# Optimization experiments

Measured on AMD Instinct MI355X. Metric: run time of the kernel, lower is better.

Reference implementation:

```python
import jax, jax.numpy as jnp
import numpy as np

N = 100_000   # num destination nodes (adj rows)
M = 100_000   # num source/neighbor nodes (adj cols)
E = 3_200_000 # num edges (avg degree 32)
D_IN = 128
DIM = 128
LEAKY_ALPHA = 0.2  # tf.nn.leaky_relu default


def setup_inputs() -> dict:
    key = jax.random.key(0)
    ks = jax.random.split(key, 7)
    return {
        "self_embedding": jax.random.normal(ks[0], (N, D_IN), jnp.float32),
        "neigh_embedding": jax.random.normal(ks[1], (M, D_IN), jnp.float32),
        "W": jax.random.normal(ks[2], (D_IN, DIM), jnp.float32) / np.sqrt(D_IN).astype(np.float32),
        "w_self": jax.random.normal(ks[3], (DIM, 1), jnp.float32) * 0.1,
        "w_neigh": jax.random.normal(ks[4], (DIM, 1), jnp.float32) * 0.1,
        "edge_row": jax.random.randint(ks[5], (E,), 0, N, jnp.int32),
        "edge_col": jax.random.randint(ks[6], (E,), 0, M, jnp.int32),
    }


def reference(self_embedding, neigh_embedding, W, w_self, w_neigh, edge_row, edge_col):
    # Dense projections (shared weight, no bias)
    from_all = neigh_embedding @ W    # [M, DIM]
    from_self = self_embedding @ W    # [N, DIM]

    # Per-node attention logits
    self_weight = (from_self @ w_self)[:, 0]   # [N]
    all_weight = (from_all @ w_neigh)[:, 0]    # [M]

    # Per-edge score: leaky_relu(self_weight[row] + all_weight[col])
    scores = jax.nn.leaky_relu(self_weight[edge_row] + all_weight[edge_col],
                               negative_slope=LEAKY_ALPHA)  # [E]

    n = self_embedding.shape[0]
    # Sparse (segment) softmax over each row's edges, numerically stable
    row_max = jax.ops.segment_max(scores, edge_row, num_segments=n)
    row_max = jnp.where(jnp.isfinite(row_max), row_max, 0.0)  # guard empty rows
    e = jnp.exp(scores - row_max[edge_row])
    denom = jax.ops.segment_sum(e, edge_row, num_segments=n)
    denom = jnp.where(denom > 0, denom, 1.0)
    alpha = e / denom[edge_row]  # [E]

    # Sparse-dense matmul: output[i] = sum_j alpha_ij * from_all[j]
    agg = jax.ops.segment_sum(alpha[:, None] * from_all[edge_col], edge_row,
                              num_segments=n)  # [N, DIM]

    # renorm=False path: residual with from_self, then activation
    return jax.nn.relu(from_self + agg)
```

## Files before the change

### kernel.cpp

```cpp
#include <hip/hip_runtime.h>
#include <math.h>

#define DIM 128
#define LEAKY 0.2f
#define CAP 80
#define RPB 128
#define NBMAX 1024
#define PART_CHUNK 4096

typedef __attribute__((ext_vector_type(8))) short short8_t;
typedef __attribute__((ext_vector_type(8))) __bf16 bf16x8;
typedef __attribute__((ext_vector_type(4))) float f32x4;

__device__ __forceinline__ unsigned short f32_to_bf16_bits(float x) {
  unsigned u = __float_as_uint(x);
  u += 0x7fffu + ((u >> 16) & 1u);
  return (unsigned short)(u >> 16);
}

__global__ __launch_bounds__(256) void gemm_neigh_q(
    const float* __restrict__ emb, const float* __restrict__ W,
    const float* __restrict__ wvec, unsigned char* __restrict__ fa_i8,
    float2* __restrict__ awsc, int nrows)
{
  __shared__ __align__(16) char smem[34816];
  unsigned short* Wt = (unsigned short*)smem;
  int t = threadIdx.x;
  int lane = t & 63;
  int wid = t >> 6;

  for (int i = t; i < 4096; i += 256) {
    int k = i >> 5;
    int c4 = (i & 31) << 2;
    float4 w4 = *(const float4*)(W + k * 128 + c4);
    Wt[(c4 + 0) * 136 + k] = f32_to_bf16_bits(w4.x);
    Wt[(c4 + 1) * 136 + k] = f32_to_bf16_bits(w4.y);
    Wt[(c4 + 2) * 136 + k] = f32_to_bf16_bits(w4.z);
    Wt[(c4 + 3) * 136 + k] = f32_to_bf16_bits(w4.w);
  }
  __syncthreads();

  int row0 = blockIdx.x * 128 + wid * 32;
  bool active = row0 < nrows;
  int lr = lane & 15;
  int lk = lane >> 4;

  f32x4 acc[2][8];
  if (active) {
    bf16x8 a[2][4];
#pragma unroll
    for (int rf = 0; rf < 2; rf++) {
      int row = row0 + rf * 16 + lr;
      row = min(row, nrows - 1);
      const float* src = emb + (size_t)row * DIM;
#pragma unroll
      for (int ks = 0; ks < 4; ks++) {
        int kb = ks * 32 + lk * 8;
        float4 x = *(const float4*)(src + kb);
        float4 y = *(const float4*)(src + kb + 4);
        union { short8_t s; bf16x8 b; } f;
        f.s[0] = (short)f32_to_bf16_bits(x.x); f.s[1] = (short)f32_to_bf16_bits(x.y);
        f.s[2] = (short)f32_to_bf16_bits(x.z); f.s[3] = (short)f32_to_bf16_bits(x.w);
        f.s[4] = (short)f32_to_bf16_bits(y.x); f.s[5] = (short)f32_to_bf16_bits(y.y);
        f.s[6] = (short)f32_to_bf16_bits(y.z); f.s[7] = (short)f32_to_bf16_bits(y.w);
        a[rf][ks] = f.b;
      }
    }
#pragma unroll
    for (int rf = 0; rf < 2; rf++)
#pragma unroll
      for (int cf = 0; cf < 8; cf++)
        acc[rf][cf] = (f32x4){0.f, 0.f, 0.f, 0.f};
#pragma unroll
    for (int ks = 0; ks < 4; ks++) {
#pragma unroll
      for (int cf = 0; cf < 8; cf++) {
        bf16x8 wf = *(const bf16x8*)(Wt + (cf * 16 + lr) * 136 + ks * 32 + lk * 8);
        acc[0][cf] = __builtin_amdgcn_mfma_f32_16x16x32_bf16(a[0][ks], wf, acc[0][cf], 0, 0, 0);
        acc[1][cf] = __builtin_amdgcn_mfma_f32_16x16x32_bf16(a[1][ks], wf, acc[1][cf], 0, 0, 0);
      }
    }
  }
  __syncthreads();

  unsigned char* Q = (unsigned char*)smem + wid * 4096;
  if (active) {
#pragma unroll
    for (int rf = 0; rf < 2; rf++) {
      float pp[4] = {0.f, 0.f, 0.f, 0.f};
#pragma unroll
      for (int cf = 0; cf < 8; cf++) {
        float wvv = wvec[cf * 16 + lr];
#pragma unroll
        for (int r = 0; r < 4; r++) pp[r] += acc[rf][cf][r] * wvv;
      }
#pragma unroll
      for (int r = 0; r < 4; r++) {
        pp[r] += __shfl_xor(pp[r], 1);
        pp[r] += __shfl_xor(pp[r], 2);
        pp[r] += __shfl_xor(pp[r], 4);
        pp[r] += __shfl_xor(pp[r], 8);
      }
      float m[4];
#pragma unroll
      for (int r = 0; r < 4; r++) {
        float mm = 0.f;
#pragma unroll
        for (int cf = 0; cf < 8; cf++) mm = fmaxf(mm, fabsf(acc[rf][cf][r]));
        mm = fmaxf(mm, __shfl_xor(mm, 1));
        mm = fmaxf(mm, __shfl_xor(mm, 2));
        mm = fmaxf(mm, __shfl_xor(mm, 4));
        mm = fmaxf(mm, __shfl_xor(mm, 8));
        m[r] = mm;
      }
#pragma unroll
      for (int r = 0; r < 4; r++) {
        int rl = rf * 16 + lk * 4 + r;
        int row = row0 + rl;
        float inv = m[r] > 0.f ? 127.f / m[r] : 0.f;
        if (row < nrows && lr == 0)
          awsc[row] = make_float2(pp[r], m[r] * (1.f / 127.f));
#pragma unroll
        for (int cf = 0; cf < 8; cf++) {
          int q = (int)__builtin_rintf(acc[rf][cf][r] * inv) + 128;
          Q[rl * 128 + cf * 16 + lr] = (unsigned char)(q & 0xff);
        }
      }
    }
  }
  __syncthreads();

  if (active) {
    unsigned char* dstb = fa_i8 + (size_t)row0 * DIM;
    int nbytes = min(32, nrows - row0) * DIM;
    for (int i = lane * 16; i < 4096; i += 1024) {
      if (i < nbytes)
        *(uint4*)(dstb + i) = *(const uint4*)(Q + i);
    }
  }
}

__global__ __launch_bounds__(256) void gemm_self_f32(
    const float* __restrict__ emb, const float* __restrict__ W,
    const float* __restrict__ wvec, float* __restrict__ out,
    float* __restrict__ wout, int nrows)
{
  __shared__ unsigned short Wt[128 * 136];
  int t = threadIdx.x;
  int lane = t & 63;
  int wid = t >> 6;

  for (int i = t; i < 4096; i += 256) {
    int k = i >> 5;
    int c4 = (i & 31) << 2;
    float4 w4 = *(const float4*)(W + k * 128 + c4);
    Wt[(c4 + 0) * 136 + k] = f32_to_bf16_bits(w4.x);
    Wt[(c4 + 1) * 136 + k] = f32_to_bf16_bits(w4.y);
    Wt[(c4 + 2) * 136 + k] = f32_to_bf16_bits(w4.z);
    Wt[(c4 + 3) * 136 + k] = f32_to_bf16_bits(w4.w);
  }
  __syncthreads();

  int row0 = blockIdx.x * 128 + wid * 32;
  if (row0 >= nrows) return;

  int lr = lane & 15;
  int lk = lane >> 4;

  bf16x8 a[2][4];
#pragma unroll
  for (int rf = 0; rf < 2; rf++) {
    int row = row0 + rf * 16 + lr;
    row = min(row, nrows - 1);
    const float* src = emb + (size_t)row * DIM;
#pragma unroll
    for (int ks = 0; ks < 4; ks++) {
      int kb = ks * 32 + lk * 8;
      float4 x = *(const float4*)(src + kb);
      float4 y = *(const float4*)(src + kb + 4);
      union { short8_t s; bf16x8 b; } f;
      f.s[0] = (short)f32_to_bf16_bits(x.x); f.s[1] = (short)f32_to_bf16_bits(x.y);
      f.s[2] = (short)f32_to_bf16_bits(x.z); f.s[3] = (short)f32_to_bf16_bits(x.w);
      f.s[4] = (short)f32_to_bf16_bits(y.x); f.s[5] = (short)f32_to_bf16_bits(y.y);
      f.s[6] = (short)f32_to_bf16_bits(y.z); f.s[7] = (short)f32_to_bf16_bits(y.w);
      a[rf][ks] = f.b;
    }
  }

  f32x4 acc[2][8];
#pragma unroll
  for (int rf = 0; rf < 2; rf++)
#pragma unroll
    for (int cf = 0; cf < 8; cf++)
      acc[rf][cf] = (f32x4){0.f, 0.f, 0.f, 0.f};

#pragma unroll
  for (int ks = 0; ks < 4; ks++) {
#pragma unroll
    for (int cf = 0; cf < 8; cf++) {
      bf16x8 wf = *(const bf16x8*)(Wt + (cf * 16 + lr) * 136 + ks * 32 + lk * 8);
      acc[0][cf] = __builtin_amdgcn_mfma_f32_16x16x32_bf16(a[0][ks], wf, acc[0][cf], 0, 0, 0);
      acc[1][cf] = __builtin_amdgcn_mfma_f32_16x16x32_bf16(a[1][ks], wf, acc[1][cf], 0, 0, 0);
    }
  }

#pragma unroll
  for (int rf = 0; rf < 2; rf++) {
    float pp[4] = {0.f, 0.f, 0.f, 0.f};
#pragma unroll
    for (int cf = 0; cf < 8; cf++) {
      float wvv = wvec[cf * 16 + lr];
#pragma unroll
      for (int r = 0; r < 4; r++) pp[r] += acc[rf][cf][r] * wvv;
    }
#pragma unroll
    for (int r = 0; r < 4; r++) {
      pp[r] += __shfl_xor(pp[r], 1);
      pp[r] += __shfl_xor(pp[r], 2);
      pp[r] += __shfl_xor(pp[r], 4);
      pp[r] += __shfl_xor(pp[r], 8);
    }
#pragma unroll
    for (int r = 0; r < 4; r++) {
      int row = row0 + rf * 16 + lk * 4 + r;
      if (row < nrows) {
        if (lr == 0) wout[row] = pp[r];
#pragma unroll
        for (int cf = 0; cf < 8; cf++)
          out[(size_t)row * DIM + cf * 16 + lr] = acc[rf][cf][r];
      }
    }
  }
}

__global__ __launch_bounds__(256) void partition_edges(
    const int* __restrict__ erow, const int* __restrict__ ecol,
    unsigned* __restrict__ streams, int capB, int* __restrict__ gcur,
    int E, int nb)
{
  __shared__ int cnt[NBMAX];
  __shared__ int base_[NBMAX];
  __shared__ int pos[NBMAX];
  int t = threadIdx.x;
  for (int i = t; i < nb; i += 256) { cnt[i] = 0; pos[i] = 0; }
  __syncthreads();

  int e0 = blockIdx.x * PART_CHUNK + t * 16;
  int rows[16], cols[16];
#pragma unroll
  for (int q = 0; q < 4; q++) {
    int e = e0 + q * 4;
    if (e + 3 < E) {
      *(int4*)(rows + q * 4) = *(const int4*)(erow + e);
      *(int4*)(cols + q * 4) = *(const int4*)(ecol + e);
    } else {
#pragma unroll
      for (int j = 0; j < 4; j++) {
        rows[q * 4 + j] = (e + j < E) ? erow[e + j] : -1;
        cols[q * 4 + j] = (e + j < E) ? ecol[e + j] : 0;
      }
    }
  }
#pragma unroll
  for (int j = 0; j < 16; j++)
    if (rows[j] >= 0) atomicAdd(&cnt[rows[j] >> 7], 1);
  __syncthreads();
  for (int i = t; i < nb; i += 256)
    base_[i] = cnt[i] ? atomicAdd(gcur + i, cnt[i]) : 0;
  __syncthreads();
#pragma unroll
  for (int j = 0; j < 16; j++) {
    if (rows[j] >= 0) {
      int b = rows[j] >> 7;
      int idx = base_[b] + atomicAdd(&pos[b], 1);
      if (idx < capB)
        streams[(size_t)b * capB + idx] =
            (unsigned)cols[j] | ((unsigned)(rows[j] & (RPB - 1)) << 20);
    }
  }
}

__global__ __launch_bounds__(256) void bucket_scatter(
    const unsigned* __restrict__ streams, int capB,
    const int* __restrict__ gcur,
    const float* __restrict__ sw, const float2* __restrict__ awsc,
    unsigned* __restrict__ perm, int* __restrict__ deg,
    float* __restrict__ invd, int N)
{
  __shared__ __align__(16) unsigned slots[RPB * CAP];
  __shared__ int cnt[RPB];
  __shared__ float dsum[RPB];
  __shared__ float sw_l[RPB];
  int b = blockIdx.x;
  int t = threadIdx.x;
  int row0 = b * RPB;
  if (t < RPB) {
    cnt[t] = 0; dsum[t] = 0.f;
    int row = row0 + t;
    sw_l[t] = (row < N) ? sw[row] : 0.f;
  }
  __syncthreads();

  int n = min(gcur[b], capB);
  const unsigned* s = streams + (size_t)b * capB;
  for (int i = t * 4; i < n; i += 1024) {
    int nv = min(4, n - i);
    unsigned v[4];
    if (nv == 4) {
      uint4 u = *(const uint4*)(s + i);
      v[0] = u.x; v[1] = u.y; v[2] = u.z; v[3] = u.w;
    } else {
      for (int j = 0; j < nv; j++) v[j] = s[i + j];
    }
    unsigned col[4]; int rl[4]; float2 ws[4];
#pragma unroll
    for (int j = 0; j < 4; j++) {
      if (j < nv) {
        col[j] = v[j] & 0xFFFFFu;
        rl[j] = v[j] >> 20;
        ws[j] = awsc[col[j]];
      }
    }
#pragma unroll
    for (int j = 0; j < 4; j++) {
      if (j < nv) {
        float sc = sw_l[rl[j]] + ws[j].x;
        sc = sc > 0.f ? sc : LEAKY * sc;
        float e = __expf(sc);
        atomicAdd(&dsum[rl[j]], e);
        float a = e * ws[j].y;
        unsigned eb = f32_to_bf16_bits(a);
        int p = atomicAdd(&cnt[rl[j]], 1);
        if (p < CAP) slots[rl[j] * CAP + p] = col[j] | (eb << 17);
      }
    }
  }
  __syncthreads();

  unsigned* dst = perm + (size_t)row0 * CAP;
  const int W4 = CAP / 4;
  for (int i = t; i < RPB * W4; i += 256) {
    int rl = i / W4, w = i - rl * W4;
    if (w * 4 < min(cnt[rl], CAP))
      *(uint4*)(dst + rl * CAP + w * 4) = *(const uint4*)(slots + rl * CAP + w * 4);
  }
  if (t < RPB) {
    int row = row0 + t;
    if (row < N) {
      deg[row] = min(cnt[t], CAP);
      float d = dsum[t];
      invd[row] = d > 0.f ? 1.f / d : 1.f;
    }
  }
}

__global__ __launch_bounds__(256) void aggregate_kernel(
    const unsigned char* __restrict__ fa_i8,
    const unsigned* __restrict__ perm, const int* __restrict__ deg_arr,
    const float* __restrict__ invd, float* __restrict__ out, int n)
{
  int wid = threadIdx.x >> 6;
  int lane = threadIdx.x & 63;
  int row = blockIdx.x * 4 + wid;
  if (row >= n) return;
  int deg = deg_arr[row];
  float inv = invd[row];
  size_t base = (size_t)row * CAP;

  int g  = lane >> 3;
  int sl = lane & 7;

  size_t o = (size_t)row * DIM + sl * 16;
  float4 rr0, rr1, rr2, rr3;
  if (g == 0) {
    rr0 = *(const float4*)(out + o);
    rr1 = *(const float4*)(out + o + 4);
    rr2 = *(const float4*)(out + o + 8);
    rr3 = *(const float4*)(out + o + 12);
  }

  float acc[16];
#pragma unroll
  for (int k = 0; k < 16; k++) acc[k] = 0.f;
  float Bl = 0.f;

  for (int bb = 0; bb < deg; bb += 64) {
    int nact = min(64, deg - bb);
    unsigned v = 0;
    if (lane < nact) v = perm[base + bb + lane];

    for (int half = 0; half < 2; half++) {
      if (half * 32 >= nact) break;
#pragma unroll
      for (int jj = 0; jj < 4; jj++) {
        int eidx = half * 32 + (jj << 3) + g;
        unsigned vj = __shfl(v, eidx);
        int   cj = vj & 0x1FFFFu;
        float aj = __uint_as_float((vj >> 17) << 16);
        uint4 u = *(const uint4*)(fa_i8 + (size_t)cj * DIM + sl * 16);
        Bl += aj;
        acc[0]  += aj * (float)( u.x        & 0xffu);
        acc[1]  += aj * (float)((u.x >> 8 ) & 0xffu);
        acc[2]  += aj * (float)((u.x >> 16) & 0xffu);
        acc[3]  += aj * (float)( u.x >> 24);
        acc[4]  += aj * (float)( u.y        & 0xffu);
        acc[5]  += aj * (float)((u.y >> 8 ) & 0xffu);
        acc[6]  += aj * (float)((u.y >> 16) & 0xffu);
        acc[7]  += aj * (float)( u.y >> 24);
        acc[8]  += aj * (float)( u.z        & 0xffu);
        acc[9]  += aj * (float)((u.z >> 8 ) & 0xffu);
        acc[10] += aj * (float)((u.z >> 16) & 0xffu);
        acc[11] += aj * (float)( u.z >> 24);
        acc[12] += aj * (float)( u.w        & 0xffu);
        acc[13] += aj * (float)((u.w >> 8 ) & 0xffu);
        acc[14] += aj * (float)((u.w >> 16) & 0xffu);
        acc[15] += aj * (float)( u.w >> 24);
      }
    }
  }

  Bl += __shfl_xor(Bl, 8); Bl += __shfl_xor(Bl, 16); Bl += __shfl_xor(Bl, 32);
#pragma unroll
  for (int k = 0; k < 16; k++) {
    acc[k] += __shfl_xor(acc[k], 8);
    acc[k] += __shfl_xor(acc[k], 16);
    acc[k] += __shfl_xor(acc[k], 32);
  }
  float B = -128.f * Bl;

  if (g == 0) {
    float r[16] = {rr0.x, rr0.y, rr0.z, rr0.w, rr1.x, rr1.y, rr1.z, rr1.w,
                   rr2.x, rr2.y, rr2.z, rr2.w, rr3.x, rr3.y, rr3.z, rr3.w};
#pragma unroll
    for (int k = 0; k < 16; k++) {
      float x = r[k] + (acc[k] + B) * inv;
      r[k] = x > 0.f ? x : 0.f;
    }
    *(float4*)(out + o)      = make_float4(r[0],  r[1],  r[2],  r[3]);
    *(float4*)(out + o + 4)  = make_float4(r[4],  r[5],  r[6],  r[7]);
    *(float4*)(out + o + 8)  = make_float4(r[8],  r[9],  r[10], r[11]);
    *(float4*)(out + o + 12) = make_float4(r[12], r[13], r[14], r[15]);
  }
}

extern "C" void kernel_launch(void* const* d_in, const int* in_sizes, int n_in,
                              void* d_out, int out_size, void* d_ws, size_t ws_size,
                              hipStream_t stream)
{
  const float* self_emb  = (const float*)d_in[0];
  const float* neigh_emb = (const float*)d_in[1];
  const float* W         = (const float*)d_in[2];
  const float* w_self    = (const float*)d_in[3];
  const float* w_neigh   = (const float*)d_in[4];
  const int*   erow      = (const int*)d_in[5];
  const int*   ecol      = (const int*)d_in[6];

  const int N = in_sizes[0] / DIM;
  const int M = in_sizes[1] / DIM;
  const int E = in_sizes[5];

  float* out = (float*)d_out;

  char* ws = (char*)d_ws;
  size_t off = 0;
  auto alloc = [&](size_t bytes) -> char* {
    char* p = ws + off;
    off += (bytes + 255) & ~(size_t)255;
    return p;
  };
  unsigned char* fa_i8  = (unsigned char*)alloc((size_t)M * DIM);
  float2* awsc  = (float2*)alloc((size_t)M * sizeof(float2));
  float* self_w = (float*)alloc((size_t)N * sizeof(float));
  int*   deg    = (int*)alloc((size_t)N * sizeof(int));
  float* invd   = (float*)alloc((size_t)N * sizeof(float));
  int*   gcur   = (int*)alloc(NBMAX * sizeof(int));
  unsigned* perm = (unsigned*)alloc((size_t)N * CAP * sizeof(unsigned));

  const int nb = (N + RPB - 1) / RPB;
  const int capB = (E / nb + 1024 + 3) & ~3;
  unsigned* streams = (unsigned*)alloc((size_t)nb * capB * sizeof(unsigned));

  hipMemsetAsync(gcur, 0, nb * sizeof(int), stream);

  gemm_neigh_q<<<(M + 127) / 128, 256, 0, stream>>>(neigh_emb, W, w_neigh,
                                                    fa_i8, awsc, M);

  gemm_self_f32<<<(N + 127) / 128, 256, 0, stream>>>(self_emb, W, w_self,
                                                     out, self_w, N);

  int pblocks = (E + PART_CHUNK - 1) / PART_CHUNK;
  partition_edges<<<pblocks, 256, 0, stream>>>(erow, ecol, streams, capB, gcur, E, nb);

  bucket_scatter<<<nb, 256, 0, stream>>>(streams, capB, gcur, self_w, awsc,
                                         perm, deg, invd, N);

  aggregate_kernel<<<(N + 3) / 4, 256, 0, stream>>>(fa_i8, perm, deg, invd, out, N);
}
```

Baseline: 250.3 us.

## Move awsc gather into partition pass and pack bf16 weights into edge stream

The random gather of per-column attention weights (awsc) moves from bucket_scatter into partition_edges, where the column indices are already loaded. Both values are packed as bf16 into the upper half of a 64-bit stream entry, so bucket_scatter reads them straight from the bucket stream. This takes dependent random loads out of the latency-bound scatter kernel, but it doubles the stream write and read traffic and rounds the attention logit to bf16 before the exponential. bucket_scatter also drops its 4-wide vector load in favour of one 64-bit load per thread.

```diff
diff --git a/kernel.cpp b/kernel.cpp
--- a/kernel.cpp
+++ b/kernel.cpp
@@ -16,6 +16,9 @@
   unsigned u = __float_as_uint(x);
   u += 0x7fffu + ((u >> 16) & 1u);
   return (unsigned short)(u >> 16);
+}
+__device__ __forceinline__ float bf16_bits_to_f32(unsigned b) {
+  return __uint_as_float(b << 16);
 }
 
 __global__ __launch_bounds__(256) void gemm_neigh_q(
@@ -235,8 +238,9 @@
 
 __global__ __launch_bounds__(256) void partition_edges(
     const int* __restrict__ erow, const int* __restrict__ ecol,
-    unsigned* __restrict__ streams, int capB, int* __restrict__ gcur,
-    int E, int nb)
+    const float2* __restrict__ awsc,
+    unsigned long long* __restrict__ streams, int capB,
+    int* __restrict__ gcur, int E, int nb)
 {
   __shared__ int cnt[NBMAX];
   __shared__ int base_[NBMAX];
@@ -268,22 +272,30 @@
   for (int i = t; i < nb; i += 256)
     base_[i] = cnt[i] ? atomicAdd(gcur + i, cnt[i]) : 0;
   __syncthreads();
+
+  float2 ws[16];
+#pragma unroll
+  for (int j = 0; j < 16; j++)
+    ws[j] = awsc[cols[j]];
+
 #pragma unroll
   for (int j = 0; j < 16; j++) {
     if (rows[j] >= 0) {
       int b = rows[j] >> 7;
       int idx = base_[b] + atomicAdd(&pos[b], 1);
-      if (idx < capB)
-        streams[(size_t)b * capB + idx] =
-            (unsigned)cols[j] | ((unsigned)(rows[j] & (RPB - 1)) << 20);
+      if (idx < capB) {
+        unsigned lo = (unsigned)cols[j] | ((unsigned)(rows[j] & (RPB - 1)) << 20);
+        unsigned hi = ((unsigned)f32_to_bf16_bits(ws[j].x) << 16) |
+                      (unsigned)f32_to_bf16_bits(ws[j].y);
+        streams[(size_t)b * capB + idx] = ((unsigned long long)hi << 32) | lo;
+      }
     }
   }
 }
 
 __global__ __launch_bounds__(256) void bucket_scatter(
-    const unsigned* __restrict__ streams, int capB,
-    const int* __restrict__ gcur,
-    const float* __restrict__ sw, const float2* __restrict__ awsc,
+    const unsigned long long* __restrict__ streams, int capB,
+    const int* __restrict__ gcur, const float* __restrict__ sw,
     unsigned* __restrict__ perm, int* __restrict__ deg,
     float* __restrict__ invd, int N)
 {
@@ -302,38 +314,23 @@
   __syncthreads();
 
   int n = min(gcur[b], capB);
-  const unsigned* s = streams + (size_t)b * capB;
-  for (int i = t * 4; i < n; i += 1024) {
-    int nv = min(4, n - i);
-    unsigned v[4];
-    if (nv == 4) {
-      uint4 u = *(const uint4*)(s + i);
-      v[0] = u.x; v[1] = u.y; v[2] = u.z; v[3] = u.w;
-    } else {
-      for (int j = 0; j < nv; j++) v[j] = s[i + j];
-    }
-    unsigned col[4]; int rl[4]; float2 ws[4];
-#pragma unroll
-    for (int j = 0; j < 4; j++) {
-      if (j < nv) {
-        col[j] = v[j] & 0xFFFFFu;
-        rl[j] = v[j] >> 20;
-        ws[j] = awsc[col[j]];
-      }
-    }
-#pragma unroll
-    for (int j = 0; j < 4; j++) {
-      if (j < nv) {
-        float sc = sw_l[rl[j]] + ws[j].x;
-        sc = sc > 0.f ? sc : LEAKY * sc;
-        float e = __expf(sc);
-        atomicAdd(&dsum[rl[j]], e);
-        float a = e * ws[j].y;
-        unsigned eb = f32_to_bf16_bits(a);
-        int p = atomicAdd(&cnt[rl[j]], 1);
-        if (p < CAP) slots[rl[j] * CAP + p] = col[j] | (eb << 17);
-      }
-    }
+  const unsigned long long* s = streams + (size_t)b * capB;
+  for (int i = t; i < n; i += 256) {
+    unsigned long long v = s[i];
+    unsigned lo = (unsigned)v;
+    unsigned hi = (unsigned)(v >> 32);
+    int rl = (lo >> 20) & (RPB - 1);
+    unsigned col = lo & 0xFFFFFu;
+    float aw = bf16_bits_to_f32(hi >> 16);
+    float sc = bf16_bits_to_f32(hi & 0xffffu);
+    float s2 = sw_l[rl] + aw;
+    s2 = s2 > 0.f ? s2 : LEAKY * s2;
+    float e = __expf(s2);
+    atomicAdd(&dsum[rl], e);
+    float a = e * sc;
+    unsigned ab = f32_to_bf16_bits(a);
+    int p = atomicAdd(&cnt[rl], 1);
+    if (p < CAP) slots[rl * CAP + p] = col | (ab << 17);
   }
   __syncthreads();
 
@@ -478,7 +475,8 @@
 
   const int nb = (N + RPB - 1) / RPB;
   const int capB = (E / nb + 1024 + 3) & ~3;
-  unsigned* streams = (unsigned*)alloc((size_t)nb * capB * sizeof(unsigned));
+  unsigned long long* streams =
+      (unsigned long long*)alloc((size_t)nb * capB * sizeof(unsigned long long));
 
   hipMemsetAsync(gcur, 0, nb * sizeof(int), stream);
 
@@ -489,9 +487,10 @@
                                                      out, self_w, N);
 
   int pblocks = (E + PART_CHUNK - 1) / PART_CHUNK;
-  partition_edges<<<pblocks, 256, 0, stream>>>(erow, ecol, streams, capB, gcur, E, nb);
-
-  bucket_scatter<<<nb, 256, 0, stream>>>(streams, capB, gcur, self_w, awsc,
+  partition_edges<<<pblocks, 256, 0, stream>>>(erow, ecol, awsc, streams, capB,
+                                               gcur, E, nb);
+
+  bucket_scatter<<<nb, 256, 0, stream>>>(streams, capB, gcur, self_w,
                                          perm, deg, invd, N);
 
   aggregate_kernel<<<(N + 3) / 4, 256, 0, stream>>>(fa_i8, perm, deg, invd, out, N);
```

Result: no change. 254.5 us (+1.7%).
